# Optimization experiments

Measured on AMD Instinct MI355X. Metric: run time of the kernel, lower is better.

## Reference

```python
import jax, jax.numpy as jnp
import numpy as np


def _kabsch_rmsd(p, c):
    # p, c: [N, 3]
    pm = jnp.mean(p, axis=0)  # [3]
    cm = jnp.mean(c, axis=0)  # [3]
    # 3x3 cross-covariance
    A = (p - pm).T @ (c - cm)
    U, S, Vt = jnp.linalg.svd(A, full_matrices=False)
    d = jnp.sign(jnp.linalg.det(A))
    # corr_mat = diag([1, 1, d]);  rotation = U @ corr_mat @ Vt
    scale = jnp.concatenate([jnp.ones((2,), dtype=p.dtype), d[None].astype(p.dtype)])
    R = U @ (scale[:, None] * Vt)  # [3,3]
    # translation = pm - R @ cm; aligned coords = (R @ c^T)^T + translation
    aligned = c @ R.T + (pm - R @ cm)
    sq = jnp.sum((p - aligned) ** 2, axis=1)  # [N]
    return jnp.sqrt(jnp.mean(sq))


def setup_inputs() -> dict:
    key = jax.random.key(0)
    k1, k2 = jax.random.split(key)
    B, N = 4096, 2048
    coords_pred = jax.random.normal(k1, (B, N, 3), dtype=jnp.float32)
    coords = jax.random.normal(k2, (B, N, 3), dtype=jnp.float32)
    return {"coords_pred": coords_pred, "coords": coords}


def reference(coords_pred, coords):
    # Batched Kabsch alignment + RMSD; default mode='global', return_all=False
    # -> mean over the per-sample RMSDs.
    rmsds = jax.vmap(_kabsch_rmsd)(coords_pred, coords)  # [B]
    return jnp.mean(rmsds)
```

## Files before the change

### kernel.cpp

```cpp
#include <hip/hip_runtime.h>
#include <math.h>

#define NPTS 2048
#define BLOCK 1024
#define BPB 4
#define WPB 4

__global__ __launch_bounds__(BLOCK, 8) void kabsch_kernel(
    const float* __restrict__ P, const float* __restrict__ C,
    float* __restrict__ out, int B) {
  const int w = threadIdx.x >> 6;
  const int lane = threadIdx.x & 63;
  const int batch = blockIdx.x * BPB + (w >> 2);
  const int slice = w & 3;

  float acc[17];
#pragma unroll
  for (int i = 0; i < 17; i++) acc[i] = 0.f;

#define ACCUM(PA, PB, PQ, CA, CB, CQ)                                   \
  do {                                                                  \
    const float Px[4] = {PA.x, PA.w, PB.z, PQ.y};                       \
    const float Py[4] = {PA.y, PB.x, PB.w, PQ.z};                       \
    const float Pz[4] = {PA.z, PB.y, PQ.x, PQ.w};                       \
    const float Cx[4] = {CA.x, CA.w, CB.z, CQ.y};                       \
    const float Cy[4] = {CA.y, CB.x, CB.w, CQ.z};                       \
    const float Cz[4] = {CA.z, CB.y, CQ.x, CQ.w};                       \
    _Pragma("unroll")                                                   \
    for (int i = 0; i < 4; i++) {                                       \
      const float px = Px[i], py = Py[i], pz = Pz[i];                   \
      const float cx = Cx[i], cy = Cy[i], cz = Cz[i];                   \
      acc[0] += px; acc[1] += py; acc[2] += pz;                         \
      acc[3] += cx; acc[4] += cy; acc[5] += cz;                         \
      acc[6] += px * px + py * py + pz * pz;                            \
      acc[7] += cx * cx + cy * cy + cz * cz;                            \
      acc[8]  += px * cx; acc[9]  += px * cy; acc[10] += px * cz;       \
      acc[11] += py * cx; acc[12] += py * cy; acc[13] += py * cz;       \
      acc[14] += pz * cx; acc[15] += pz * cy; acc[16] += pz * cz;       \
    }                                                                   \
  } while (0)

  if (batch < B) {
    const float4* p4 = (const float4*)P + (size_t)batch * 1536 + slice * 384 + 3 * lane;
    const float4* c4 = (const float4*)C + (size_t)batch * 1536 + slice * 384 + 3 * lane;
#pragma unroll
    for (int it = 0; it < 2; ++it) {
      const float4 pa = p4[it * 192],     pb = p4[it * 192 + 1], pq = p4[it * 192 + 2];
      const float4 ca = c4[it * 192],     cb = c4[it * 192 + 1], cq = c4[it * 192 + 2];
      ACCUM(pa, pb, pq, ca, cb, cq);
    }
  }

#pragma unroll
  for (int off = 32; off > 0; off >>= 1) {
#pragma unroll
    for (int i = 0; i < 17; i++) acc[i] += __shfl_down(acc[i], off);
  }

  __shared__ float red[BPB * WPB][17];
  if (lane == 0) {
#pragma unroll
    for (int i = 0; i < 17; i++) red[w][i] = acc[i];
  }
  __syncthreads();

  double v = 0.0;
  if (threadIdx.x < BPB) {
    const int t = threadIdx.x;
    const int bt = blockIdx.x * BPB + t;
    if (bt < B) {
      double s[17];
#pragma unroll
      for (int i = 0; i < 17; i++) {
        float f = red[t * WPB][i];
#pragma unroll
        for (int j = 1; j < WPB; j++) f += red[t * WPB + j][i];
        s[i] = (double)f;
      }
      const double invN = 1.0 / (double)NPTS;
      const double spx = s[0], spy = s[1], spz = s[2];
      const double scx = s[3], scy = s[4], scz = s[5];
      const double Ep = s[6] - (spx * spx + spy * spy + spz * spz) * invN;
      const double Ec = s[7] - (scx * scx + scy * scy + scz * scz) * invN;
      const double a00 = s[8]  - spx * scx * invN, a01 = s[9]  - spx * scy * invN, a02 = s[10] - spx * scz * invN;
      const double a10 = s[11] - spy * scx * invN, a11 = s[12] - spy * scy * invN, a12 = s[13] - spy * scz * invN;
      const double a20 = s[14] - spz * scx * invN, a21 = s[15] - spz * scy * invN, a22 = s[16] - spz * scz * invN;
      const double det = a00 * (a11 * a22 - a12 * a21)
                       - a01 * (a10 * a22 - a12 * a20)
                       + a02 * (a10 * a21 - a11 * a20);
      const double b00 = a00 * a00 + a10 * a10 + a20 * a20;
      const double b11 = a01 * a01 + a11 * a11 + a21 * a21;
      const double b22 = a02 * a02 + a12 * a12 + a22 * a22;
      const double b01 = a00 * a01 + a10 * a11 + a20 * a21;
      const double b02 = a00 * a02 + a10 * a12 + a20 * a22;
      const double b12 = a01 * a02 + a11 * a12 + a21 * a22;
      const double q = (b00 + b11 + b22) / 3.0;
      const double p1 = b01 * b01 + b02 * b02 + b12 * b12;
      const double d0 = b00 - q, d1 = b11 - q, d2 = b22 - q;
      const double p2 = d0 * d0 + d1 * d1 + d2 * d2 + 2.0 * p1;
      double e1, e2, e3;
      if (p2 < 1e-30) {
        e1 = e2 = e3 = q;
      } else {
        const double pp = sqrt(p2 / 6.0);
        const double inv = 1.0 / pp;
        const double c00 = d0 * inv, c11 = d1 * inv, c22 = d2 * inv;
        const double c01 = b01 * inv, c02 = b02 * inv, c12 = b12 * inv;
        double r = 0.5 * (c00 * (c11 * c22 - c12 * c12)
                        - c01 * (c01 * c22 - c12 * c02)
                        + c02 * (c01 * c12 - c11 * c02));
        r = fmin(1.0, fmax(-1.0, r));
        const double phi = acos(r) / 3.0;
        e1 = q + 2.0 * pp * cos(phi);
        e3 = q + 2.0 * pp * cos(phi + 2.0943951023931953);
        e2 = 3.0 * q - e1 - e3;
      }
      const double s1 = sqrt(fmax(e1, 0.0));
      const double s2 = sqrt(fmax(e2, 0.0));
      const double s3 = sqrt(fmax(e3, 0.0));
      const double dsign = (det > 0.0) ? 1.0 : ((det < 0.0) ? -1.0 : 0.0);
      const double trRS = s1 + s2 + dsign * s3;
      const double msd = (Ep + Ec - 2.0 * trRS) * invN;
      v = sqrt(fmax(msd, 0.0));
    }
  }
  v += __shfl_down(v, 2);
  v += __shfl_down(v, 1);
  if (threadIdx.x == 0) atomicAdd(out, (float)(v / (double)B));
}

extern "C" void kernel_launch(void* const* d_in, const int* in_sizes, int n_in,
                              void* d_out, int out_size, void* d_ws, size_t ws_size,
                              hipStream_t stream) {
  const float* P = (const float*)d_in[0];
  const float* C = (const float*)d_in[1];
  float* out = (float*)d_out;
  const int B = in_sizes[0] / (NPTS * 3);
  hipMemsetAsync(out, 0, sizeof(float), stream);
  kabsch_kernel<<<(B + BPB - 1) / BPB, BLOCK, 0, stream>>>(P, C, out, B);
}
```

Before: 221.4 us.

## Use one block per batch with inline-asm batched loads and staged waits

Switches from 1024-thread blocks covering four batches to 256-thread blocks covering one batch each. Every thread now issues all twelve dwordx4 loads up front through inline assembly and waits in two stages, so accumulation on the first half overlaps the second half's loads. This aims to raise memory-level parallelism and cut block-level sync overhead. In exchange there are four times as many atomicAdds on the output, and the hand-written vmcnt waits rely on the compiler keeping the asm load order.

```diff
diff --git a/kernel.cpp b/kernel.cpp
--- a/kernel.cpp
+++ b/kernel.cpp
@@ -2,21 +2,38 @@
 #include <math.h>
 
 #define NPTS 2048
-#define BLOCK 1024
-#define BPB 4
-#define WPB 4
+#define BLOCK 256
+#define FPB (NPTS * 3)
+#define SHOT_OFF 3072
 
-__global__ __launch_bounds__(BLOCK, 8) void kabsch_kernel(
-    const float* __restrict__ P, const float* __restrict__ C,
-    float* __restrict__ out, int B) {
-  const int w = threadIdx.x >> 6;
-  const int lane = threadIdx.x & 63;
-  const int batch = blockIdx.x * BPB + (w >> 2);
-  const int slice = w & 3;
 
-  float acc[17];
-#pragma unroll
-  for (int i = 0; i < 17; i++) acc[i] = 0.f;
+#define ISSUE12(O0,O1,O2,O3,O4,O5,O6,O7,O8,O9,O10,O11, p0,c0,p1,c1)      \
+  asm volatile(                                                          \
+      "global_load_dwordx4 %0, %12, off\n\t"                             \
+      "global_load_dwordx4 %1, %12, off offset:16\n\t"                   \
+      "global_load_dwordx4 %2, %12, off offset:32\n\t"                   \
+      "global_load_dwordx4 %3, %13, off\n\t"                             \
+      "global_load_dwordx4 %4, %13, off offset:16\n\t"                   \
+      "global_load_dwordx4 %5, %13, off offset:32\n\t"                   \
+      "global_load_dwordx4 %6, %14, off\n\t"                             \
+      "global_load_dwordx4 %7, %14, off offset:16\n\t"                   \
+      "global_load_dwordx4 %8, %14, off offset:32\n\t"                   \
+      "global_load_dwordx4 %9, %15, off\n\t"                             \
+      "global_load_dwordx4 %10, %15, off offset:16\n\t"                  \
+      "global_load_dwordx4 %11, %15, off offset:32\n\t"                  \
+      : "=&v"(O0), "=&v"(O1), "=&v"(O2), "=&v"(O3), "=&v"(O4), "=&v"(O5),\
+        "=&v"(O6), "=&v"(O7), "=&v"(O8), "=&v"(O9), "=&v"(O10), "=&v"(O11)\
+      : "v"(p0), "v"(c0), "v"(p1), "v"(c1))
+
+#define TIE4(V) "+v"((V).x), "+v"((V).y), "+v"((V).z), "+v"((V).w)
+
+#define WAIT_PIN6(N, a, b, c, d, e, f)                                   \
+  do {                                                                   \
+    asm volatile("s_waitcnt vmcnt(" #N ")" ::: "memory");                \
+    asm volatile("" : TIE4(a), TIE4(b), TIE4(c));                        \
+    asm volatile("" : TIE4(d), TIE4(e), TIE4(f));                        \
+    __builtin_amdgcn_sched_barrier(0);                                   \
+  } while (0)
 
 #define ACCUM(PA, PB, PQ, CA, CB, CQ)                                   \
   do {                                                                  \
@@ -40,93 +57,106 @@
     }                                                                   \
   } while (0)
 
-  if (batch < B) {
-    const float4* p4 = (const float4*)P + (size_t)batch * 1536 + slice * 384 + 3 * lane;
-    const float4* c4 = (const float4*)C + (size_t)batch * 1536 + slice * 384 + 3 * lane;
+__device__ __forceinline__ double kabsch_epilogue(const float* sf) {
+  double s[17];
 #pragma unroll
-    for (int it = 0; it < 2; ++it) {
-      const float4 pa = p4[it * 192],     pb = p4[it * 192 + 1], pq = p4[it * 192 + 2];
-      const float4 ca = c4[it * 192],     cb = c4[it * 192 + 1], cq = c4[it * 192 + 2];
-      ACCUM(pa, pb, pq, ca, cb, cq);
-    }
+  for (int i = 0; i < 17; i++) s[i] = (double)sf[i];
+  const double invN = 1.0 / (double)NPTS;
+  const double spx = s[0], spy = s[1], spz = s[2];
+  const double scx = s[3], scy = s[4], scz = s[5];
+  const double Ep = s[6] - (spx * spx + spy * spy + spz * spz) * invN;
+  const double Ec = s[7] - (scx * scx + scy * scy + scz * scz) * invN;
+  const double a00 = s[8]  - spx * scx * invN, a01 = s[9]  - spx * scy * invN, a02 = s[10] - spx * scz * invN;
+  const double a10 = s[11] - spy * scx * invN, a11 = s[12] - spy * scy * invN, a12 = s[13] - spy * scz * invN;
+  const double a20 = s[14] - spz * scx * invN, a21 = s[15] - spz * scy * invN, a22 = s[16] - spz * scz * invN;
+  const double det = a00 * (a11 * a22 - a12 * a21)
+                   - a01 * (a10 * a22 - a12 * a20)
+                   + a02 * (a10 * a21 - a11 * a20);
+  const double b00 = a00 * a00 + a10 * a10 + a20 * a20;
+  const double b11 = a01 * a01 + a11 * a11 + a21 * a21;
+  const double b22 = a02 * a02 + a12 * a12 + a22 * a22;
+  const double b01 = a00 * a01 + a10 * a11 + a20 * a21;
+  const double b02 = a00 * a02 + a10 * a12 + a20 * a22;
+  const double b12 = a01 * a02 + a11 * a12 + a21 * a22;
+  const double q = (b00 + b11 + b22) / 3.0;
+  const double p1 = b01 * b01 + b02 * b02 + b12 * b12;
+  const double d0 = b00 - q, d1 = b11 - q, d2 = b22 - q;
+  const double p2 = d0 * d0 + d1 * d1 + d2 * d2 + 2.0 * p1;
+  double e1, e2, e3;
+  if (p2 < 1e-30) {
+    e1 = e2 = e3 = q;
+  } else {
+    const double pp = sqrt(p2 / 6.0);
+    const double inv = 1.0 / pp;
+    const double c00 = d0 * inv, c11 = d1 * inv, c22 = d2 * inv;
+    const double c01 = b01 * inv, c02 = b02 * inv, c12 = b12 * inv;
+    double r = 0.5 * (c00 * (c11 * c22 - c12 * c12)
+                    - c01 * (c01 * c22 - c12 * c02)
+                    + c02 * (c01 * c12 - c11 * c02));
+    r = fmin(1.0, fmax(-1.0, r));
+    const double phi = acos(r) / 3.0;
+    e1 = q + 2.0 * pp * cos(phi);
+    e3 = q + 2.0 * pp * cos(phi + 2.0943951023931953);
+    e2 = 3.0 * q - e1 - e3;
   }
+  const double s1 = sqrt(fmax(e1, 0.0));
+  const double s2 = sqrt(fmax(e2, 0.0));
+  const double s3 = sqrt(fmax(e3, 0.0));
+  const double dsign = (det > 0.0) ? 1.0 : ((det < 0.0) ? -1.0 : 0.0);
+  const double trRS = s1 + s2 + dsign * s3;
+  const double msd = (Ep + Ec - 2.0 * trRS) * invN;
+  return sqrt(fmax(msd, 0.0));
+}
+
+__global__ __launch_bounds__(BLOCK, 4) void kabsch_kernel(
+    const float* __restrict__ P, const float* __restrict__ C,
+    float* __restrict__ out, int B) {
+  const int t = threadIdx.x;
+  const int wave = t >> 6, lane = t & 63;
+  const int b = blockIdx.x;
+  __shared__ float red[BLOCK / 64][17];
+
+  const float* p0 = P + (size_t)b * FPB + 12 * t;
+  const float* c0 = C + (size_t)b * FPB + 12 * t;
+  const float* p1 = p0 + SHOT_OFF;
+  const float* c1 = c0 + SHOT_OFF;
+
+  float4 A0, A1, A2, A3, A4, A5, A6, A7, A8, A9, A10, A11;
+  ISSUE12(A0, A1, A2, A3, A4, A5, A6, A7, A8, A9, A10, A11,
+          p0, c0, p1, c1);
+
+  float acc[17];
+#pragma unroll
+  for (int i = 0; i < 17; i++) acc[i] = 0.f;
+
+  WAIT_PIN6(6, A0, A1, A2, A3, A4, A5);
+  ACCUM(A0, A1, A2, A3, A4, A5);
+
+  WAIT_PIN6(0, A6, A7, A8, A9, A10, A11);
+  ACCUM(A6, A7, A8, A9, A10, A11);
 
 #pragma unroll
   for (int off = 32; off > 0; off >>= 1) {
 #pragma unroll
     for (int i = 0; i < 17; i++) acc[i] += __shfl_down(acc[i], off);
   }
-
-  __shared__ float red[BPB * WPB][17];
   if (lane == 0) {
 #pragma unroll
-    for (int i = 0; i < 17; i++) red[w][i] = acc[i];
+    for (int i = 0; i < 17; i++) red[wave][i] = acc[i];
   }
   __syncthreads();
 
-  double v = 0.0;
-  if (threadIdx.x < BPB) {
-    const int t = threadIdx.x;
-    const int bt = blockIdx.x * BPB + t;
-    if (bt < B) {
-      double s[17];
+  if (t == 0) {
+    float s[17];
 #pragma unroll
-      for (int i = 0; i < 17; i++) {
-        float f = red[t * WPB][i];
+    for (int i = 0; i < 17; i++) {
+      float v = red[0][i];
 #pragma unroll
-        for (int j = 1; j < WPB; j++) f += red[t * WPB + j][i];
-        s[i] = (double)f;
-      }
-      const double invN = 1.0 / (double)NPTS;
-      const double spx = s[0], spy = s[1], spz = s[2];
-      const double scx = s[3], scy = s[4], scz = s[5];
-      const double Ep = s[6] - (spx * spx + spy * spy + spz * spz) * invN;
-      const double Ec = s[7] - (scx * scx + scy * scy + scz * scz) * invN;
-      const double a00 = s[8]  - spx * scx * invN, a01 = s[9]  - spx * scy * invN, a02 = s[10] - spx * scz * invN;
-      const double a10 = s[11] - spy * scx * invN, a11 = s[12] - spy * scy * invN, a12 = s[13] - spy * scz * invN;
-      const double a20 = s[14] - spz * scx * invN, a21 = s[15] - spz * scy * invN, a22 = s[16] - spz * scz * invN;
-      const double det = a00 * (a11 * a22 - a12 * a21)
-                       - a01 * (a10 * a22 - a12 * a20)
-                       + a02 * (a10 * a21 - a11 * a20);
-      const double b00 = a00 * a00 + a10 * a10 + a20 * a20;
-      const double b11 = a01 * a01 + a11 * a11 + a21 * a21;
-      const double b22 = a02 * a02 + a12 * a12 + a22 * a22;
-      const double b01 = a00 * a01 + a10 * a11 + a20 * a21;
-      const double b02 = a00 * a02 + a10 * a12 + a20 * a22;
-      const double b12 = a01 * a02 + a11 * a12 + a21 * a22;
-      const double q = (b00 + b11 + b22) / 3.0;
-      const double p1 = b01 * b01 + b02 * b02 + b12 * b12;
-      const double d0 = b00 - q, d1 = b11 - q, d2 = b22 - q;
-      const double p2 = d0 * d0 + d1 * d1 + d2 * d2 + 2.0 * p1;
-      double e1, e2, e3;
-      if (p2 < 1e-30) {
-        e1 = e2 = e3 = q;
-      } else {
-        const double pp = sqrt(p2 / 6.0);
-        const double inv = 1.0 / pp;
-        const double c00 = d0 * inv, c11 = d1 * inv, c22 = d2 * inv;
-        const double c01 = b01 * inv, c02 = b02 * inv, c12 = b12 * inv;
-        double r = 0.5 * (c00 * (c11 * c22 - c12 * c12)
-                        - c01 * (c01 * c22 - c12 * c02)
-                        + c02 * (c01 * c12 - c11 * c02));
-        r = fmin(1.0, fmax(-1.0, r));
-        const double phi = acos(r) / 3.0;
-        e1 = q + 2.0 * pp * cos(phi);
-        e3 = q + 2.0 * pp * cos(phi + 2.0943951023931953);
-        e2 = 3.0 * q - e1 - e3;
-      }
-      const double s1 = sqrt(fmax(e1, 0.0));
-      const double s2 = sqrt(fmax(e2, 0.0));
-      const double s3 = sqrt(fmax(e3, 0.0));
-      const double dsign = (det > 0.0) ? 1.0 : ((det < 0.0) ? -1.0 : 0.0);
-      const double trRS = s1 + s2 + dsign * s3;
-      const double msd = (Ep + Ec - 2.0 * trRS) * invN;
-      v = sqrt(fmax(msd, 0.0));
+      for (int w = 1; w < BLOCK / 64; w++) v += red[w][i];
+      s[i] = v;
     }
+    atomicAdd(out, (float)(kabsch_epilogue(s) / (double)B));
   }
-  v += __shfl_down(v, 2);
-  v += __shfl_down(v, 1);
-  if (threadIdx.x == 0) atomicAdd(out, (float)(v / (double)B));
 }
 
 extern "C" void kernel_launch(void* const* d_in, const int* in_sizes, int n_in,
@@ -135,7 +165,7 @@
   const float* P = (const float*)d_in[0];
   const float* C = (const float*)d_in[1];
   float* out = (float*)d_out;
-  const int B = in_sizes[0] / (NPTS * 3);
+  const int B = in_sizes[0] / FPB;
   hipMemsetAsync(out, 0, sizeof(float), stream);
-  kabsch_kernel<<<(B + BPB - 1) / BPB, BLOCK, 0, stream>>>(P, C, out, B);
+  kabsch_kernel<<<B, BLOCK, 0, stream>>>(P, C, out, B);
 }
```

Result: faster. 216.9 us (-2.0%).
